# Kernel optimization log

Measured on AMD Instinct MI355X. Metric: run time of the kernel, lower is better.

Reference implementation:

```python
import jax, jax.numpy as jnp
import numpy as np

T, E = 8192, 1024
LAYER_DEPTH, NUM_LAYERS = 12, 24


def _init_params():
    ratio_0_to_1 = LAYER_DEPTH / (NUM_LAYERS - 1)
    ratio_1_to_almost_0 = 1.0 - LAYER_DEPTH / NUM_LAYERS
    zigzag = 0.5 * (jnp.arange(1, E + 1) % 3 - 1)
    time_first = jnp.full(E, jnp.log(0.3), dtype=jnp.float32) + zigzag.astype(jnp.float32)
    h = jnp.arange(0, E, dtype=jnp.float32)
    time_decay = (-5 + 8 * (h / (E - 1)) ** (0.7 + 1.3 * ratio_0_to_1)).astype(jnp.float32)
    xr = jnp.arange(E, dtype=jnp.float32) / E
    time_mix_k = jnp.power(xr, ratio_1_to_almost_0)
    time_mix_v = time_mix_k + 0.3 * ratio_0_to_1
    time_mix_r = jnp.power(xr, 0.5 * ratio_1_to_almost_0)
    return time_first, time_decay, time_mix_k, time_mix_v, time_mix_r


def setup_inputs() -> dict:
    key = jax.random.key(0)
    kx, kk_, kv_, kr_, ko_ = jax.random.split(key, 5)
    scale = 1.0 / np.sqrt(E)
    tf, td, tmk, tmv, tmr = _init_params()
    return {
        "x": jax.random.normal(kx, (T, E), dtype=jnp.float32),
        "sx": jnp.zeros((E,), jnp.float32),
        "aa": jnp.zeros((E,), jnp.float32),
        "bb": jnp.zeros((E,), jnp.float32),
        "pp": jnp.zeros((E,), jnp.float32),
        "time_first": tf,
        "time_decay": td,
        "time_mix_k": tmk,
        "time_mix_v": tmv,
        "time_mix_r": tmr,
        "Wk": jax.random.normal(kk_, (E, E), jnp.float32) * scale,
        "Wv": jax.random.normal(kv_, (E, E), jnp.float32) * scale,
        "Wr": jax.random.normal(kr_, (E, E), jnp.float32) * scale,
        "Wo": jax.random.normal(ko_, (E, E), jnp.float32) * scale,
    }


def reference(x, sx, aa, bb, pp, time_first, time_decay,
              time_mix_k, time_mix_v, time_mix_r, Wk, Wv, Wr, Wo):
    # token-shift: previous token (or carried state sx at t=0)  [T, E]
    sx_seq = jnp.concatenate((sx[None, :], x[:-1, :]), axis=0)
    kx = x * time_mix_k + sx_seq * (1.0 - time_mix_k)
    vx = x * time_mix_v + sx_seq * (1.0 - time_mix_v)
    rx = x * time_mix_r + sx_seq * (1.0 - time_mix_r)

    r = jax.nn.sigmoid(rx @ Wr)  # [T, E]
    k = kx @ Wk                  # [T, E]
    v = vx @ Wv                  # [T, E]
    decay = -jnp.exp(time_decay)  # [E]

    def step(state, kv):
        aa_, bb_, pp_ = state
        kk, vv = kv
        ww = time_first + kk
        p = jnp.maximum(pp_, ww)
        e1 = jnp.exp(pp_ - p)
        e2 = jnp.exp(ww - p)
        out = (e1 * aa_ + e2 * vv) / (e1 * bb_ + e2)
        ww2 = decay + pp_
        p2 = jnp.maximum(ww2, kk)
        e1b = jnp.exp(ww2 - p2)
        e2b = jnp.exp(kk - p2)
        return (e1b * aa_ + e2b * vv, e1b * bb_ + e2b, p2), out

    (aa_f, bb_f, pp_f), wkv = jax.lax.scan(step, (aa, bb, pp), (k, v))
    out = x + (r * wkv) @ Wo
    return out, x[-1, :], aa_f, bb_f, pp_f
```

## Files before the change

kernel.cpp:

```cpp
#include <hip/hip_runtime.h>
#include <cstdint>
#include <cstddef>

typedef __bf16 bf16x8 __attribute__((ext_vector_type(8)));
typedef float  f32x4  __attribute__((ext_vector_type(4)));

#define TT 8192
#define EE 1024
#define LDSK 40

__device__ __forceinline__ unsigned short f2bf(float f) {
    union { float f; unsigned int u; } v; v.f = f;
    unsigned int r = v.u + 0x7FFFu + ((v.u >> 16) & 1u);
    return (unsigned short)(r >> 16);
}
__device__ __forceinline__ float b2f(unsigned int h) {
    union { unsigned int u; float f; } v; v.u = h << 16; return v.f;
}
__device__ __forceinline__ void gload_lds16(const void* g, void* l) {
    __builtin_amdgcn_global_load_lds((__attribute__((address_space(1))) void*)g,
                                     (__attribute__((address_space(3))) void*)l, 16, 0, 0);
}

__global__ void wt_kernel(const float* __restrict__ Wk, const float* __restrict__ Wv,
                          const float* __restrict__ Wr, const float* __restrict__ Wo,
                          unsigned short* __restrict__ Tk, unsigned short* __restrict__ Tv,
                          unsigned short* __restrict__ Tr, unsigned short* __restrict__ To) {
    __shared__ float tile[32][33];
    const float* W; unsigned short* D;
    switch (blockIdx.z) {
        case 0:  W = Wk; D = Tk; break;
        case 1:  W = Wv; D = Tv; break;
        case 2:  W = Wr; D = Tr; break;
        default: W = Wo; D = To; break;
    }
    const int bx = blockIdx.x * 32, by = blockIdx.y * 32;
    const int tx = threadIdx.x, ty = threadIdx.y;
#pragma unroll
    for (int r = 0; r < 4; ++r)
        tile[ty + 8 * r][tx] = W[(size_t)(by + ty + 8 * r) * EE + bx + tx];
    __syncthreads();
#pragma unroll
    for (int r = 0; r < 4; ++r)
        D[(size_t)(bx + ty + 8 * r) * EE + by + tx] = f2bf(tile[tx][ty + 8 * r]);
}

__global__ void prep_kernel(const float* __restrict__ Wk, const float* __restrict__ Wv,
                            const float* __restrict__ Wr, const float* __restrict__ Wo,
                            unsigned short* __restrict__ Tk, unsigned short* __restrict__ Tv,
                            unsigned short* __restrict__ Tr, unsigned short* __restrict__ To,
                            const float* __restrict__ x, const float* __restrict__ sx,
                            const float* __restrict__ tmk, const float* __restrict__ tmv,
                            const float* __restrict__ tmr,
                            unsigned short* __restrict__ kxb, unsigned short* __restrict__ vxb,
                            unsigned short* __restrict__ rxb) {
    const int bid = blockIdx.x;
    if (bid < 4096) {
        __shared__ float tile[32][33];
        const int z = bid >> 10;
        const float* W; unsigned short* D;
        switch (z) {
            case 0:  W = Wk; D = Tk; break;
            case 1:  W = Wv; D = Tv; break;
            case 2:  W = Wr; D = Tr; break;
            default: W = Wo; D = To; break;
        }
        const int by = ((bid >> 5) & 31) * 32, bx = (bid & 31) * 32;
        const int tx = threadIdx.x & 31, ty = threadIdx.x >> 5;
#pragma unroll
        for (int r = 0; r < 4; ++r)
            tile[ty + 8 * r][tx] = W[(size_t)(by + ty + 8 * r) * EE + bx + tx];
        __syncthreads();
#pragma unroll
        for (int r = 0; r < 4; ++r)
            D[(size_t)(bx + ty + 8 * r) * EE + by + tx] = f2bf(tile[tx][ty + 8 * r]);
    } else {
        const int gid  = (bid - 4096) * 256 + threadIdx.x;
        const int base = gid * 4;
        const int t = base >> 10;
        const int e = base & (EE - 1);
        float4 xv = *(const float4*)(x + base);
        float4 pv = (t > 0) ? *(const float4*)(x + base - EE) : *(const float4*)(sx + e);
        float4 mk = *(const float4*)(tmk + e);
        float4 mv = *(const float4*)(tmv + e);
        float4 mr = *(const float4*)(tmr + e);
        ushort4 ko, vo, ro;
        ko.x = f2bf(fmaf(mk.x, xv.x - pv.x, pv.x));
        ko.y = f2bf(fmaf(mk.y, xv.y - pv.y, pv.y));
        ko.z = f2bf(fmaf(mk.z, xv.z - pv.z, pv.z));
        ko.w = f2bf(fmaf(mk.w, xv.w - pv.w, pv.w));
        vo.x = f2bf(fmaf(mv.x, xv.x - pv.x, pv.x));
        vo.y = f2bf(fmaf(mv.y, xv.y - pv.y, pv.y));
        vo.z = f2bf(fmaf(mv.z, xv.z - pv.z, pv.z));
        vo.w = f2bf(fmaf(mv.w, xv.w - pv.w, pv.w));
        ro.x = f2bf(fmaf(mr.x, xv.x - pv.x, pv.x));
        ro.y = f2bf(fmaf(mr.y, xv.y - pv.y, pv.y));
        ro.z = f2bf(fmaf(mr.z, xv.z - pv.z, pv.z));
        ro.w = f2bf(fmaf(mr.w, xv.w - pv.w, pv.w));
        *(ushort4*)(kxb + base) = ko;
        *(ushort4*)(vxb + base) = vo;
        *(ushort4*)(rxb + base) = ro;
    }
}

__global__ __launch_bounds__(256, 4) void gemm_kvr3(
        const unsigned short* __restrict__ kxb, const unsigned short* __restrict__ vxb,
        const unsigned short* __restrict__ rxb,
        const unsigned short* __restrict__ Wkt, const unsigned short* __restrict__ Wvt,
        const unsigned short* __restrict__ Wrt,
        unsigned short* __restrict__ kf, unsigned short* __restrict__ vf,
        unsigned short* __restrict__ ry) {
    __shared__ __align__(16) unsigned short As[128 * 64];
    __shared__ __align__(16) unsigned short Bs[128 * 64];
    const int z = blockIdx.z;
    const unsigned short* A  = (z == 0) ? kxb : (z == 1) ? vxb : rxb;
    const unsigned short* Bt = (z == 0) ? Wkt : (z == 1) ? Wvt : Wrt;
    unsigned short* C        = (z == 0) ? kf  : (z == 1) ? vf  : ry;

    const int tid  = threadIdx.x;
    const int wave = tid >> 6, lane = tid & 63;
    const int wm = (wave >> 1) * 64, wn = (wave & 1) * 64;
    const int l15 = lane & 15, lq = lane >> 4;
    const int lrow = lane >> 3;
    const int lcolg = (((lane & 7) ^ lrow) & 7) * 8;
    const int sw = l15 & 7;
    const int bm = blockIdx.x * 128, bn = blockIdx.y * 128;

    f32x4 acc[4][4] = {};

    for (int kt = 0; kt < 1024; kt += 64) {
        __syncthreads();
#pragma unroll
        for (int p = 0; p < 4; ++p) {
            const int r0 = p * 32 + wave * 8;
            gload_lds16(A  + (size_t)(bm + r0 + lrow) * 1024 + kt + lcolg, &As[r0 * 64]);
            gload_lds16(Bt + (size_t)(bn + r0 + lrow) * 1024 + kt + lcolg, &Bs[r0 * 64]);
        }
        __syncthreads();
#pragma unroll
        for (int h = 0; h < 2; ++h) {
            bf16x8 af[4], bfr[4];
#pragma unroll
            for (int i = 0; i < 4; ++i) {
                const int g = ((h * 4 + lq) ^ sw) * 8;
                af[i]  = *(const bf16x8*)(&As[(wm + i * 16 + l15) * 64 + g]);
                bfr[i] = *(const bf16x8*)(&Bs[(wn + i * 16 + l15) * 64 + g]);
            }
#pragma unroll
            for (int i = 0; i < 4; ++i)
#pragma unroll
                for (int j = 0; j < 4; ++j)
                    acc[i][j] = __builtin_amdgcn_mfma_f32_16x16x32_bf16(af[i], bfr[j], acc[i][j], 0, 0, 0);
        }
    }

    const bool sig = (z == 2);
#pragma unroll
    for (int i = 0; i < 4; ++i)
#pragma unroll
        for (int j = 0; j < 4; ++j) {
            const int col = bn + wn + j * 16 + l15;
#pragma unroll
            for (int r = 0; r < 4; ++r) {
                const int row = bm + wm + i * 16 + lq * 4 + r;
                float val = acc[i][j][r];
                if (sig) val = 1.f / (1.f + __expf(-val));
                C[(size_t)row * 1024 + col] = f2bf(val);
            }
        }
}

__global__ __launch_bounds__(256, 4) void gemm_wo(const unsigned short* __restrict__ A,
                                                  const unsigned short* __restrict__ Bt,
                                                  const float* __restrict__ Res,
                                                  float* __restrict__ C) {
    __shared__ __align__(16) unsigned short As[128 * 64];
    __shared__ __align__(16) unsigned short Bs[128 * 64];
    const int tid  = threadIdx.x;
    const int wave = tid >> 6, lane = tid & 63;
    const int wm = (wave >> 1) * 64, wn = (wave & 1) * 64;
    const int l15 = lane & 15, lq = lane >> 4;
    const int lrow = lane >> 3;
    const int lcolg = (((lane & 7) ^ lrow) & 7) * 8;
    const int sw = l15 & 7;
    const int bm = blockIdx.x * 128, bn = blockIdx.y * 128;

    f32x4 acc[4][4] = {};

    for (int kt = 0; kt < 1024; kt += 64) {
        __syncthreads();
#pragma unroll
        for (int p = 0; p < 4; ++p) {
            const int r0 = p * 32 + wave * 8;
            gload_lds16(A  + (size_t)(bm + r0 + lrow) * 1024 + kt + lcolg, &As[r0 * 64]);
            gload_lds16(Bt + (size_t)(bn + r0 + lrow) * 1024 + kt + lcolg, &Bs[r0 * 64]);
        }
        __syncthreads();
#pragma unroll
        for (int h = 0; h < 2; ++h) {
            bf16x8 af[4], bfr[4];
#pragma unroll
            for (int i = 0; i < 4; ++i) {
                const int g = ((h * 4 + lq) ^ sw) * 8;
                af[i]  = *(const bf16x8*)(&As[(wm + i * 16 + l15) * 64 + g]);
                bfr[i] = *(const bf16x8*)(&Bs[(wn + i * 16 + l15) * 64 + g]);
            }
#pragma unroll
            for (int i = 0; i < 4; ++i)
#pragma unroll
                for (int j = 0; j < 4; ++j)
                    acc[i][j] = __builtin_amdgcn_mfma_f32_16x16x32_bf16(af[i], bfr[j], acc[i][j], 0, 0, 0);
        }
    }

#pragma unroll
    for (int i = 0; i < 4; ++i)
#pragma unroll
        for (int j = 0; j < 4; ++j) {
            const int col = bn + wn + j * 16 + l15;
#pragma unroll
            for (int r = 0; r < 4; ++r) {
                const int row = bm + wm + i * 16 + lq * 4 + r;
                const size_t idx = (size_t)row * 1024 + col;
                C[idx] = acc[i][j][r] + Res[idx];
            }
        }
}

template <int NC>
__global__ void wkv_pass_a(const unsigned short* __restrict__ k,
                           const unsigned short* __restrict__ v,
                           const float* __restrict__ td,
                           float* __restrict__ Sa, float* __restrict__ Sb, float* __restrict__ Sp) {
    const int CL = TT / NC;
    const int gid = blockIdx.x * 256 + threadIdx.x;
    const int c  = gid >> 8;
    const int e0 = (gid & 255) * 4;
    const float4 tdv = *(const float4*)(td + e0);
    float w[4] = { -__expf(tdv.x), -__expf(tdv.y), -__expf(tdv.z), -__expf(tdv.w) };
    float sa[4] = {0.f, 0.f, 0.f, 0.f}, sb[4] = {0.f, 0.f, 0.f, 0.f};
    float sp[4] = {-1e30f, -1e30f, -1e30f, -1e30f};
    const size_t base = (size_t)c * CL * EE + e0;
#pragma unroll
    for (int i = 0; i < CL; ++i) {
        const ushort4 k4 = *(const ushort4*)(k + base + (size_t)i * EE);
        const ushort4 v4 = *(const ushort4*)(v + base + (size_t)i * EE);
        const unsigned short ks[4] = {k4.x, k4.y, k4.z, k4.w};
        const unsigned short vs[4] = {v4.x, v4.y, v4.z, v4.w};
        const float fi = (float)(CL - 1 - i);
#pragma unroll
        for (int j = 0; j < 4; ++j) {
            const float kk = b2f(ks[j]), vv = b2f(vs[j]);
            const float q  = fmaf(w[j], fi, kk);
            const float p2 = fmaxf(sp[j], q);
            const float e1 = __expf(sp[j] - p2), e2 = __expf(q - p2);
            sa[j] = fmaf(e1, sa[j], e2 * vv);
            sb[j] = fmaf(e1, sb[j], e2);
            sp[j] = p2;
        }
    }
#pragma unroll
    for (int j = 0; j < 4; ++j) {
        Sa[c * EE + e0 + j] = sa[j];
        Sb[c * EE + e0 + j] = sb[j];
        Sp[c * EE + e0 + j] = sp[j];
    }
}

template <int NC>
__global__ void wkv_pass_b_par(const float* __restrict__ aa, const float* __restrict__ bb,
                               const float* __restrict__ pp, const float* __restrict__ td,
                               const float* __restrict__ x,
                               const float* __restrict__ Sa, const float* __restrict__ Sb,
                               const float* __restrict__ Sp,
                               float* __restrict__ ina, float* __restrict__ inb,
                               float* __restrict__ inp, float* __restrict__ outTail) {
    const int CL = TT / NC;
    const int e = blockIdx.x, c = threadIdx.x;
    __shared__ float sA[NC], sB[NC], sP[NC];
    const float w = -__expf(td[e]);

    float a = Sa[c * EE + e], b = Sb[c * EE + e], p = Sp[c * EE + e];

    for (int s = 1; s < NC; s <<= 1) {
        sA[c] = a; sB[c] = b; sP[c] = p;
        __syncthreads();
        if (c >= s) {
            const float myLen = (float)(CL * min(c + 1, s));
            const float aL = sA[c - s], bL = sB[c - s], pL = sP[c - s];
            const float pLd = pL + w * myLen;
            const float pn  = fmaxf(pLd, p);
            const float e1  = __expf(pLd - pn), e2 = __expf(p - pn);
            a = fmaf(e1, aL, e2 * a);
            b = fmaf(e1, bL, e2 * b);
            p = pn;
        }
        __syncthreads();
    }

    sA[c] = a; sB[c] = b; sP[c] = p;
    __syncthreads();

    const float a0 = aa[e], b0 = bb[e], p0 = pp[e];
    float ea, eb, ep;
    if (c == 0) { ea = a0; eb = b0; ep = p0; }
    else {
        const float aL = sA[c - 1], bL = sB[c - 1], pL = sP[c - 1];
        const float p0d = p0 + w * (float)(c * CL);
        const float pn  = fmaxf(p0d, pL);
        const float e1  = __expf(p0d - pn), e2 = __expf(pL - pn);
        ea = fmaf(e1, a0, e2 * aL);
        eb = fmaf(e1, b0, e2 * bL);
        ep = pn;
    }
    ina[e * NC + c] = ea; inb[e * NC + c] = eb; inp[e * NC + c] = ep;

    if (c == NC - 1) {
        const float p0d = p0 + w * (float)TT;
        const float pn  = fmaxf(p0d, p);
        const float e1  = __expf(p0d - pn), e2 = __expf(p - pn);
        outTail[e]          = x[(size_t)(TT - 1) * EE + e];
        outTail[EE + e]     = fmaf(e1, a0, e2 * a);
        outTail[2 * EE + e] = fmaf(e1, b0, e2 * b);
        outTail[3 * EE + e] = pn;
    }
}

template <int NC>
__global__ void wkv_pass_c(const unsigned short* __restrict__ k,
                           const unsigned short* __restrict__ v,
                           const float* __restrict__ tf, const float* __restrict__ td,
                           const float* __restrict__ ina, const float* __restrict__ inb,
                           const float* __restrict__ inp,
                           unsigned short* ry) {
    const int CL = TT / NC;
    const int gid = blockIdx.x * 256 + threadIdx.x;
    const int c  = gid >> 8;
    const int e0 = (gid & 255) * 4;
    const float4 tdv = *(const float4*)(td + e0);
    const float4 tfv = *(const float4*)(tf + e0);
    float w[4] = { -__expf(tdv.x), -__expf(tdv.y), -__expf(tdv.z), -__expf(tdv.w) };
    float u[4] = { tfv.x, tfv.y, tfv.z, tfv.w };
    float a[4], b[4], p[4];
#pragma unroll
    for (int j = 0; j < 4; ++j) {
        a[j] = ina[(e0 + j) * NC + c];
        b[j] = inb[(e0 + j) * NC + c];
        p[j] = inp[(e0 + j) * NC + c];
    }
    const size_t base = (size_t)c * CL * EE + e0;
#pragma unroll 4
    for (int i = 0; i < CL; ++i) {
        const size_t idx = base + (size_t)i * EE;
        const ushort4 k4 = *(const ushort4*)(k + idx);
        const ushort4 v4 = *(const ushort4*)(v + idx);
        const ushort4 r4 = *(const ushort4*)(ry + idx);
        const unsigned short ks[4] = {k4.x, k4.y, k4.z, k4.w};
        const unsigned short vs[4] = {v4.x, v4.y, v4.z, v4.w};
        const unsigned short rs[4] = {r4.x, r4.y, r4.z, r4.w};
        unsigned short os[4];
#pragma unroll
        for (int j = 0; j < 4; ++j) {
            const float kk = b2f(ks[j]), vv = b2f(vs[j]), rr = b2f(rs[j]);
            const float ww = u[j] + kk;
            const float pq = fmaxf(p[j], ww);
            const float e1 = __expf(p[j] - pq), e2 = __expf(ww - pq);
            const float wkv = fmaf(e1, a[j], e2 * vv) * __builtin_amdgcn_rcpf(fmaf(e1, b[j], e2));
            os[j] = f2bf(rr * wkv);
            const float ww2 = w[j] + p[j];
            const float p2  = fmaxf(ww2, kk);
            const float e1b = __expf(ww2 - p2), e2b = __expf(kk - p2);
            a[j] = fmaf(e1b, a[j], e2b * vv);
            b[j] = fmaf(e1b, b[j], e2b);
            p[j] = p2;
        }
        ushort4 o4;
        o4.x = os[0]; o4.y = os[1]; o4.z = os[2]; o4.w = os[3];
        *(ushort4*)(ry + idx) = o4;
    }
}

__global__ void wkv_pass_b_small(const float* __restrict__ aa, const float* __restrict__ bb,
                                 const float* __restrict__ pp, const float* __restrict__ td,
                                 const float* __restrict__ x,
                                 const float* __restrict__ Sa, const float* __restrict__ Sb,
                                 const float* __restrict__ Sp,
                                 float* __restrict__ ina, float* __restrict__ inb,
                                 float* __restrict__ inp, float* __restrict__ outTail) {
    const int NC = 128, CL = TT / NC;
    const int e = blockIdx.x * 256 + threadIdx.x;
    const float w  = -__expf(td[e]);
    const float wL = w * (float)CL;
    float a = aa[e], b = bb[e], p = pp[e];
    for (int c = 0; c < NC; ++c) {
        ina[e * NC + c] = a; inb[e * NC + c] = b; inp[e * NC + c] = p;
        const int idx = c * EE + e;
        const float sa = Sa[idx], sb = Sb[idx], sp = Sp[idx];
        const float pw = p + wL;
        const float p2 = fmaxf(pw, sp);
        const float e1 = __expf(pw - p2), e2 = __expf(sp - p2);
        a = fmaf(e1, a, e2 * sa);
        b = fmaf(e1, b, e2 * sb);
        p = p2;
    }
    outTail[e]          = x[(size_t)(TT - 1) * EE + e];
    outTail[EE + e]     = a;
    outTail[2 * EE + e] = b;
    outTail[3 * EE + e] = p;
}

__global__ __launch_bounds__(256, 4) void gemm_kvr(
        const float* __restrict__ X, const float* __restrict__ SX,
        const float* __restrict__ tmk, const float* __restrict__ tmv,
        const float* __restrict__ tmr,
        const unsigned short* __restrict__ Wkt, const unsigned short* __restrict__ Wvt,
        const unsigned short* __restrict__ Wrt,
        unsigned short* __restrict__ outK, unsigned short* __restrict__ outV,
        unsigned short* __restrict__ outR) {
    __shared__ __align__(16) unsigned short As[128 * LDSK];
    __shared__ __align__(16) unsigned short Bs[128 * LDSK];
    const int z = blockIdx.z;
    const float* TM = (z == 0) ? tmk : (z == 1) ? tmv : tmr;
    const unsigned short* Bt = (z == 0) ? Wkt : (z == 1) ? Wvt : Wrt;
    unsigned short* Cout = (z == 0) ? outK : (z == 1) ? outV : outR;

    const int tid  = threadIdx.x;
    const int wave = tid >> 6, lane = tid & 63;
    const int wm = (wave >> 1) * 64, wn = (wave & 1) * 64;
    const int l15 = lane & 15, lq = lane >> 4;
    const int bm = blockIdx.x * 128, bn = blockIdx.y * 128;

    f32x4 acc[4][4] = {};

    for (int kt = 0; kt < 1024; kt += 32) {
        __syncthreads();
#pragma unroll
        for (int p = 0; p < 2; ++p) {
            const int li  = p * 256 + tid;
            const int row = li >> 2, q = li & 3;
            const int e0  = kt + q * 8;
            {
                const int t = bm + row;
                const float* xr = X + (size_t)t * EE + e0;
                const float* pr = (t > 0) ? (X + (size_t)(t - 1) * EE + e0) : (SX + e0);
                float4 xa = *(const float4*)xr, xb = *(const float4*)(xr + 4);
                float4 pa = *(const float4*)pr, pb = *(const float4*)(pr + 4);
                float4 ma = *(const float4*)(TM + e0), mb = *(const float4*)(TM + e0 + 4);
                ushort4 lo, hi;
                lo.x = f2bf(fmaf(ma.x, xa.x - pa.x, pa.x));
                lo.y = f2bf(fmaf(ma.y, xa.y - pa.y, pa.y));
                lo.z = f2bf(fmaf(ma.z, xa.z - pa.z, pa.z));
                lo.w = f2bf(fmaf(ma.w, xa.w - pa.w, pa.w));
                hi.x = f2bf(fmaf(mb.x, xb.x - pb.x, pb.x));
                hi.y = f2bf(fmaf(mb.y, xb.y - pb.y, pb.y));
                hi.z = f2bf(fmaf(mb.z, xb.z - pb.z, pb.z));
                hi.w = f2bf(fmaf(mb.w, xb.w - pb.w, pb.w));
                *(ushort4*)(&As[row * LDSK + q * 8])     = lo;
                *(ushort4*)(&As[row * LDSK + q * 8 + 4]) = hi;
            }
            *(uint4*)(&Bs[row * LDSK + q * 8]) =
                *(const uint4*)(Bt + (size_t)(bn + row) * 1024 + e0);
        }
        __syncthreads();
        bf16x8 af[4], bfr[4];
#pragma unroll
        for (int i = 0; i < 4; ++i) {
            af[i]  = *(const bf16x8*)(&As[(wm + i * 16 + l15) * LDSK + lq * 8]);
            bfr[i] = *(const bf16x8*)(&Bs[(wn + i * 16 + l15) * LDSK + lq * 8]);
        }
#pragma unroll
        for (int i = 0; i < 4; ++i)
#pragma unroll
            for (int j = 0; j < 4; ++j)
                acc[i][j] = __builtin_amdgcn_mfma_f32_16x16x32_bf16(af[i], bfr[j], acc[i][j], 0, 0, 0);
    }

    const bool sig = (z == 2);
#pragma unroll
    for (int i = 0; i < 4; ++i)
#pragma unroll
        for (int j = 0; j < 4; ++j) {
            const int col = bn + wn + j * 16 + l15;
#pragma unroll
            for (int r = 0; r < 4; ++r) {
                const int row = bm + wm + i * 16 + lq * 4 + r;
                float val = acc[i][j][r];
                if (sig) val = 1.f / (1.f + __expf(-val));
                Cout[(size_t)row * 1024 + col] = f2bf(val);
            }
        }
}

extern "C" void kernel_launch(void* const* d_in, const int* in_sizes, int n_in,
                              void* d_out, int out_size, void* d_ws, size_t ws_size,
                              hipStream_t stream) {
    const float* x   = (const float*)d_in[0];
    const float* sx  = (const float*)d_in[1];
    const float* aa  = (const float*)d_in[2];
    const float* bb  = (const float*)d_in[3];
    const float* pp  = (const float*)d_in[4];
    const float* tf  = (const float*)d_in[5];
    const float* td  = (const float*)d_in[6];
    const float* tmk = (const float*)d_in[7];
    const float* tmv = (const float*)d_in[8];
    const float* tmr = (const float*)d_in[9];
    const float* Wk  = (const float*)d_in[10];
    const float* Wv  = (const float*)d_in[11];
    const float* Wr  = (const float*)d_in[12];
    const float* Wo  = (const float*)d_in[13];
    float* out = (float*)d_out;

    char* ws = (char*)d_ws;
    const size_t MB = 1ull << 20;

    unsigned short* Wkt = (unsigned short*)(ws + 0 * MB);
    unsigned short* Wvt = (unsigned short*)(ws + 2 * MB);
    unsigned short* Wrt = (unsigned short*)(ws + 4 * MB);
    unsigned short* Wot = (unsigned short*)(ws + 6 * MB);

    if (ws_size >= 75 * MB) {
        unsigned short* rxb = (unsigned short*)(ws + 8 * MB);
        unsigned short* kf  = (unsigned short*)(ws + 24 * MB);
        unsigned short* ry  = (unsigned short*)(ws + 40 * MB);
        unsigned short* vf  = (unsigned short*)(ws + 56 * MB);
        float* Sa  = (float*)(ws + 8  * MB);
        float* Sb  = (float*)(ws + 10 * MB);
        float* Sp  = (float*)(ws + 12 * MB);
        float* ina = (float*)(ws + 14 * MB);
        float* inb = (float*)(ws + 16 * MB);
        float* inp = (float*)(ws + 18 * MB);
        unsigned short* kxb = (unsigned short*)d_out;
        unsigned short* vxb = (unsigned short*)d_out + (size_t)TT * EE;

        prep_kernel<<<12288, 256, 0, stream>>>(Wk, Wv, Wr, Wo, Wkt, Wvt, Wrt, Wot,
                                               x, sx, tmk, tmv, tmr, kxb, vxb, rxb);
        gemm_kvr3<<<dim3(64, 8, 3), 256, 0, stream>>>(kxb, vxb, rxb, Wkt, Wvt, Wrt,
                                                      kf, vf, ry);
        wkv_pass_a<512><<<512, 256, 0, stream>>>(kf, vf, td, Sa, Sb, Sp);
        wkv_pass_b_par<512><<<EE, 512, 0, stream>>>(aa, bb, pp, td, x, Sa, Sb, Sp,
                                                    ina, inb, inp, out + (size_t)TT * EE);
        wkv_pass_c<512><<<512, 256, 0, stream>>>(kf, vf, tf, td,
                                                 ina, inb, inp, ry);
        gemm_wo<<<dim3(64, 8), 256, 0, stream>>>(ry, Wot, x, out);
    } else {
        unsigned short* ry = (unsigned short*)(ws + 8 * MB);
        char* scan = ws + 24 * MB;
        const size_t QK = (size_t)128 * EE * sizeof(float);
        float* Sa  = (float*)(scan);
        float* Sb  = (float*)(scan + QK);
        float* Sp  = (float*)(scan + 2 * QK);
        float* ina = (float*)(scan + 3 * QK);
        float* inb = (float*)(scan + 4 * QK);
        float* inp = (float*)(scan + 5 * QK);
        unsigned short* kf = (unsigned short*)d_out;
        unsigned short* vf = (unsigned short*)d_out + (size_t)TT * EE;

        wt_kernel<<<dim3(32, 32, 4), dim3(32, 8), 0, stream>>>(Wk, Wv, Wr, Wo, Wkt, Wvt, Wrt, Wot);
        gemm_kvr<<<dim3(64, 8, 3), 256, 0, stream>>>(x, sx, tmk, tmv, tmr,
                                                     Wkt, Wvt, Wrt, kf, vf, ry);
        wkv_pass_a<128><<<128, 256, 0, stream>>>(kf, vf, td, Sa, Sb, Sp);
        wkv_pass_b_small<<<4, 256, 0, stream>>>(aa, bb, pp, td, x, Sa, Sb, Sp,
                                                ina, inb, inp, out + (size_t)TT * EE);
        wkv_pass_c<128><<<128, 256, 0, stream>>>(kf, vf, tf, td,
                                                 ina, inb, inp, ry);
        gemm_wo<<<dim3(64, 8), 256, 0, stream>>>(ry, Wot, x, out);
    }
}
```

Before: 257.0 us.

## Fuse three WKV scan passes into one cooperative kernel with grid sync

Replaces the three chunked-scan kernels (local chunk reduction, cross-chunk prefix, chunk replay) with one cooperative kernel that uses grid-wide syncs between phases. The k/v chunk is kept in LDS so the replay phase does not reload it from global memory. The prefix phase now has each block handle two channels with a 256-thread scan over paired chunks. This removes two launches and the k/v re-read, at the cost of two grid barriers and 64KB of LDS per block, which limits residency and requires all 512 blocks to be co-resident.

```diff
diff --git a/kernel.cpp b/kernel.cpp
--- a/kernel.cpp
+++ b/kernel.cpp
@@ -1,6 +1,9 @@
 #include <hip/hip_runtime.h>
+#include <hip/hip_cooperative_groups.h>
 #include <cstdint>
 #include <cstddef>
+
+namespace cg = cooperative_groups;
 
 typedef __bf16 bf16x8 __attribute__((ext_vector_type(8)));
 typedef float  f32x4  __attribute__((ext_vector_type(4)));
@@ -227,6 +230,180 @@
         }
 }
 
+__global__ __launch_bounds__(256, 2) void wkv_fused(
+        const unsigned short* __restrict__ kf, const unsigned short* __restrict__ vf,
+        const float* __restrict__ aa, const float* __restrict__ bb,
+        const float* __restrict__ pp, const float* __restrict__ tf,
+        const float* __restrict__ td, const float* __restrict__ x,
+        unsigned short* __restrict__ ry,
+        float* __restrict__ Sa, float* __restrict__ Sb, float* __restrict__ Sp,
+        float* __restrict__ ina, float* __restrict__ inb, float* __restrict__ inp,
+        float* __restrict__ outTail) {
+    const int NC = 512, CL = 16;
+    __shared__ __align__(16) unsigned short kL[16 * EE];
+    __shared__ __align__(16) unsigned short vL[16 * EE];
+    __shared__ float sA[256], sB[256], sP[256];
+    const int c = blockIdx.x, tid = threadIdx.x;
+    const int e0 = tid * 4;
+
+    const float4 tdv = *(const float4*)(td + e0);
+    float w4[4] = { -__expf(tdv.x), -__expf(tdv.y), -__expf(tdv.z), -__expf(tdv.w) };
+    float sa[4] = {0.f, 0.f, 0.f, 0.f}, sb[4] = {0.f, 0.f, 0.f, 0.f};
+    float sp[4] = {-1e30f, -1e30f, -1e30f, -1e30f};
+    const size_t gbase = (size_t)c * CL * EE + e0;
+#pragma unroll
+    for (int i = 0; i < CL; ++i) {
+        const ushort4 k4 = *(const ushort4*)(kf + gbase + (size_t)i * EE);
+        const ushort4 v4 = *(const ushort4*)(vf + gbase + (size_t)i * EE);
+        *(ushort4*)(kL + i * EE + e0) = k4;
+        *(ushort4*)(vL + i * EE + e0) = v4;
+        const unsigned short ks[4] = {k4.x, k4.y, k4.z, k4.w};
+        const unsigned short vs[4] = {v4.x, v4.y, v4.z, v4.w};
+        const float fi = (float)(CL - 1 - i);
+#pragma unroll
+        for (int j = 0; j < 4; ++j) {
+            const float kk = b2f(ks[j]), vv = b2f(vs[j]);
+            const float q  = fmaf(w4[j], fi, kk);
+            const float p2 = fmaxf(sp[j], q);
+            const float e1 = __expf(sp[j] - p2), e2 = __expf(q - p2);
+            sa[j] = fmaf(e1, sa[j], e2 * vv);
+            sb[j] = fmaf(e1, sb[j], e2);
+            sp[j] = p2;
+        }
+    }
+#pragma unroll
+    for (int j = 0; j < 4; ++j) {
+        Sa[(size_t)(e0 + j) * NC + c] = sa[j];
+        Sb[(size_t)(e0 + j) * NC + c] = sb[j];
+        Sp[(size_t)(e0 + j) * NC + c] = sp[j];
+    }
+    __threadfence();
+    cg::this_grid().sync();
+
+    for (int ch = 0; ch < 2; ++ch) {
+        const int e = 2 * c + ch;
+        const float w = -__expf(td[e]);
+        const float2 a2 = *(const float2*)(Sa + (size_t)e * NC + 2 * tid);
+        const float2 b2 = *(const float2*)(Sb + (size_t)e * NC + 2 * tid);
+        const float2 p2 = *(const float2*)(Sp + (size_t)e * NC + 2 * tid);
+        const float eA = a2.x, eB = b2.x, eP = p2.x;
+        float Pa, Pb, Pp;
+        {
+            const float pl = p2.x + w * (float)CL;
+            const float pn = fmaxf(pl, p2.y);
+            const float x1 = __expf(pl - pn), x2 = __expf(p2.y - pn);
+            Pa = fmaf(x1, a2.x, x2 * a2.y);
+            Pb = fmaf(x1, b2.x, x2 * b2.y);
+            Pp = pn;
+        }
+        for (int s = 1; s < 256; s <<= 1) {
+            sA[tid] = Pa; sB[tid] = Pb; sP[tid] = Pp;
+            __syncthreads();
+            if (tid >= s) {
+                const float pL = sP[tid - s] + w * (float)(CL * 2 * s);
+                const float pn = fmaxf(pL, Pp);
+                const float x1 = __expf(pL - pn), x2 = __expf(Pp - pn);
+                Pa = fmaf(x1, sA[tid - s], x2 * Pa);
+                Pb = fmaf(x1, sB[tid - s], x2 * Pb);
+                Pp = pn;
+            }
+            __syncthreads();
+        }
+        sA[tid] = Pa; sB[tid] = Pb; sP[tid] = Pp;
+        __syncthreads();
+
+        const float a0 = aa[e], b0 = bb[e], p0 = pp[e];
+        {
+            const int cc = 2 * tid;
+            float ea, eb, ep;
+            if (tid == 0) { ea = a0; eb = b0; ep = p0; }
+            else {
+                const float aP = sA[tid - 1], bP = sB[tid - 1], pP = sP[tid - 1];
+                const float p0d = p0 + w * (float)(cc * CL);
+                const float pn  = fmaxf(p0d, pP);
+                const float x1  = __expf(p0d - pn), x2 = __expf(pP - pn);
+                ea = fmaf(x1, a0, x2 * aP);
+                eb = fmaf(x1, b0, x2 * bP);
+                ep = pn;
+            }
+            ina[(size_t)cc * EE + e] = ea;
+            inb[(size_t)cc * EE + e] = eb;
+            inp[(size_t)cc * EE + e] = ep;
+        }
+        {
+            float qa, qb, qp;
+            if (tid == 0) { qa = eA; qb = eB; qp = eP; }
+            else {
+                const float pL = sP[tid - 1] + w * (float)CL;
+                const float pn = fmaxf(pL, eP);
+                const float x1 = __expf(pL - pn), x2 = __expf(eP - pn);
+                qa = fmaf(x1, sA[tid - 1], x2 * eA);
+                qb = fmaf(x1, sB[tid - 1], x2 * eB);
+                qp = pn;
+            }
+            const int cc = 2 * tid + 1;
+            const float p0d = p0 + w * (float)(cc * CL);
+            const float pn  = fmaxf(p0d, qp);
+            const float x1  = __expf(p0d - pn), x2 = __expf(qp - pn);
+            ina[(size_t)cc * EE + e] = fmaf(x1, a0, x2 * qa);
+            inb[(size_t)cc * EE + e] = fmaf(x1, b0, x2 * qb);
+            inp[(size_t)cc * EE + e] = pn;
+        }
+        if (tid == 255) {
+            const float p0d = p0 + w * (float)TT;
+            const float pn  = fmaxf(p0d, Pp);
+            const float x1  = __expf(p0d - pn), x2 = __expf(Pp - pn);
+            outTail[e]          = x[(size_t)(TT - 1) * EE + e];
+            outTail[EE + e]     = fmaf(x1, a0, x2 * Pa);
+            outTail[2 * EE + e] = fmaf(x1, b0, x2 * Pb);
+            outTail[3 * EE + e] = pn;
+        }
+        __syncthreads();
+    }
+    __threadfence();
+    cg::this_grid().sync();
+
+    const float4 tfv = *(const float4*)(tf + e0);
+    const float u[4] = { tfv.x, tfv.y, tfv.z, tfv.w };
+    float a[4], b[4], p[4];
+    {
+        const float4 av = *(const float4*)(ina + (size_t)c * EE + e0);
+        const float4 bv = *(const float4*)(inb + (size_t)c * EE + e0);
+        const float4 pv = *(const float4*)(inp + (size_t)c * EE + e0);
+        a[0] = av.x; a[1] = av.y; a[2] = av.z; a[3] = av.w;
+        b[0] = bv.x; b[1] = bv.y; b[2] = bv.z; b[3] = bv.w;
+        p[0] = pv.x; p[1] = pv.y; p[2] = pv.z; p[3] = pv.w;
+    }
+#pragma unroll 4
+    for (int i = 0; i < CL; ++i) {
+        const ushort4 k4 = *(const ushort4*)(kL + i * EE + e0);
+        const ushort4 v4 = *(const ushort4*)(vL + i * EE + e0);
+        const ushort4 r4 = *(const ushort4*)(ry + gbase + (size_t)i * EE);
+        const unsigned short ks[4] = {k4.x, k4.y, k4.z, k4.w};
+        const unsigned short vs[4] = {v4.x, v4.y, v4.z, v4.w};
+        const unsigned short rs[4] = {r4.x, r4.y, r4.z, r4.w};
+        unsigned short os[4];
+#pragma unroll
+        for (int j = 0; j < 4; ++j) {
+            const float kk = b2f(ks[j]), vv = b2f(vs[j]), rr = b2f(rs[j]);
+            const float ww = u[j] + kk;
+            const float pq = fmaxf(p[j], ww);
+            const float e1 = __expf(p[j] - pq), e2 = __expf(ww - pq);
+            const float wkv = fmaf(e1, a[j], e2 * vv) * __builtin_amdgcn_rcpf(fmaf(e1, b[j], e2));
+            os[j] = f2bf(rr * wkv);
+            const float ww2 = w4[j] + p[j];
+            const float pz  = fmaxf(ww2, kk);
+            const float e1b = __expf(ww2 - pz), e2b = __expf(kk - pz);
+            a[j] = fmaf(e1b, a[j], e2b * vv);
+            b[j] = fmaf(e1b, b[j], e2b);
+            p[j] = pz;
+        }
+        ushort4 o4;
+        o4.x = os[0]; o4.y = os[1]; o4.z = os[2]; o4.w = os[3];
+        *(ushort4*)(ry + gbase + (size_t)i * EE) = o4;
+    }
+}
+
 template <int NC>
 __global__ void wkv_pass_a(const unsigned short* __restrict__ k,
                            const unsigned short* __restrict__ v,
@@ -264,119 +441,6 @@
         Sa[c * EE + e0 + j] = sa[j];
         Sb[c * EE + e0 + j] = sb[j];
         Sp[c * EE + e0 + j] = sp[j];
-    }
-}
-
-template <int NC>
-__global__ void wkv_pass_b_par(const float* __restrict__ aa, const float* __restrict__ bb,
-                               const float* __restrict__ pp, const float* __restrict__ td,
-                               const float* __restrict__ x,
-                               const float* __restrict__ Sa, const float* __restrict__ Sb,
-                               const float* __restrict__ Sp,
-                               float* __restrict__ ina, float* __restrict__ inb,
-                               float* __restrict__ inp, float* __restrict__ outTail) {
-    const int CL = TT / NC;
-    const int e = blockIdx.x, c = threadIdx.x;
-    __shared__ float sA[NC], sB[NC], sP[NC];
-    const float w = -__expf(td[e]);
-
-    float a = Sa[c * EE + e], b = Sb[c * EE + e], p = Sp[c * EE + e];
-
-    for (int s = 1; s < NC; s <<= 1) {
-        sA[c] = a; sB[c] = b; sP[c] = p;
-        __syncthreads();
-        if (c >= s) {
-            const float myLen = (float)(CL * min(c + 1, s));
-            const float aL = sA[c - s], bL = sB[c - s], pL = sP[c - s];
-            const float pLd = pL + w * myLen;
-            const float pn  = fmaxf(pLd, p);
-            const float e1  = __expf(pLd - pn), e2 = __expf(p - pn);
-            a = fmaf(e1, aL, e2 * a);
-            b = fmaf(e1, bL, e2 * b);
-            p = pn;
-        }
-        __syncthreads();
-    }
-
-    sA[c] = a; sB[c] = b; sP[c] = p;
-    __syncthreads();
-
-    const float a0 = aa[e], b0 = bb[e], p0 = pp[e];
-    float ea, eb, ep;
-    if (c == 0) { ea = a0; eb = b0; ep = p0; }
-    else {
-        const float aL = sA[c - 1], bL = sB[c - 1], pL = sP[c - 1];
-        const float p0d = p0 + w * (float)(c * CL);
-        const float pn  = fmaxf(p0d, pL);
-        const float e1  = __expf(p0d - pn), e2 = __expf(pL - pn);
-        ea = fmaf(e1, a0, e2 * aL);
-        eb = fmaf(e1, b0, e2 * bL);
-        ep = pn;
-    }
-    ina[e * NC + c] = ea; inb[e * NC + c] = eb; inp[e * NC + c] = ep;
-
-    if (c == NC - 1) {
-        const float p0d = p0 + w * (float)TT;
-        const float pn  = fmaxf(p0d, p);
-        const float e1  = __expf(p0d - pn), e2 = __expf(p - pn);
-        outTail[e]          = x[(size_t)(TT - 1) * EE + e];
-        outTail[EE + e]     = fmaf(e1, a0, e2 * a);
-        outTail[2 * EE + e] = fmaf(e1, b0, e2 * b);
-        outTail[3 * EE + e] = pn;
-    }
-}
-
-template <int NC>
-__global__ void wkv_pass_c(const unsigned short* __restrict__ k,
-                           const unsigned short* __restrict__ v,
-                           const float* __restrict__ tf, const float* __restrict__ td,
-                           const float* __restrict__ ina, const float* __restrict__ inb,
-                           const float* __restrict__ inp,
-                           unsigned short* ry) {
-    const int CL = TT / NC;
-    const int gid = blockIdx.x * 256 + threadIdx.x;
-    const int c  = gid >> 8;
-    const int e0 = (gid & 255) * 4;
-    const float4 tdv = *(const float4*)(td + e0);
-    const float4 tfv = *(const float4*)(tf + e0);
-    float w[4] = { -__expf(tdv.x), -__expf(tdv.y), -__expf(tdv.z), -__expf(tdv.w) };
-    float u[4] = { tfv.x, tfv.y, tfv.z, tfv.w };
-    float a[4], b[4], p[4];
-#pragma unroll
-    for (int j = 0; j < 4; ++j) {
-        a[j] = ina[(e0 + j) * NC + c];
-        b[j] = inb[(e0 + j) * NC + c];
-        p[j] = inp[(e0 + j) * NC + c];
-    }
-    const size_t base = (size_t)c * CL * EE + e0;
-#pragma unroll 4
-    for (int i = 0; i < CL; ++i) {
-        const size_t idx = base + (size_t)i * EE;
-        const ushort4 k4 = *(const ushort4*)(k + idx);
-        const ushort4 v4 = *(const ushort4*)(v + idx);
-        const ushort4 r4 = *(const ushort4*)(ry + idx);
-        const unsigned short ks[4] = {k4.x, k4.y, k4.z, k4.w};
-        const unsigned short vs[4] = {v4.x, v4.y, v4.z, v4.w};
-        const unsigned short rs[4] = {r4.x, r4.y, r4.z, r4.w};
-        unsigned short os[4];
-#pragma unroll
-        for (int j = 0; j < 4; ++j) {
-            const float kk = b2f(ks[j]), vv = b2f(vs[j]), rr = b2f(rs[j]);
-            const float ww = u[j] + kk;
-            const float pq = fmaxf(p[j], ww);
-            const float e1 = __expf(p[j] - pq), e2 = __expf(ww - pq);
-            const float wkv = fmaf(e1, a[j], e2 * vv) * __builtin_amdgcn_rcpf(fmaf(e1, b[j], e2));
-            os[j] = f2bf(rr * wkv);
-            const float ww2 = w[j] + p[j];
-            const float p2  = fmaxf(ww2, kk);
-            const float e1b = __expf(ww2 - p2), e2b = __expf(kk - p2);
-            a[j] = fmaf(e1b, a[j], e2b * vv);
-            b[j] = fmaf(e1b, b[j], e2b);
-            p[j] = p2;
-        }
-        ushort4 o4;
-        o4.x = os[0]; o4.y = os[1]; o4.z = os[2]; o4.w = os[3];
-        *(ushort4*)(ry + idx) = o4;
     }
 }
 
@@ -409,6 +473,60 @@
     outTail[3 * EE + e] = p;
 }
 
+template <int NC>
+__global__ void wkv_pass_c(const unsigned short* __restrict__ k,
+                           const unsigned short* __restrict__ v,
+                           const float* __restrict__ tf, const float* __restrict__ td,
+                           const float* __restrict__ ina, const float* __restrict__ inb,
+                           const float* __restrict__ inp,
+                           unsigned short* ry) {
+    const int CL = TT / NC;
+    const int gid = blockIdx.x * 256 + threadIdx.x;
+    const int c  = gid >> 8;
+    const int e0 = (gid & 255) * 4;
+    const float4 tdv = *(const float4*)(td + e0);
+    const float4 tfv = *(const float4*)(tf + e0);
+    float w[4] = { -__expf(tdv.x), -__expf(tdv.y), -__expf(tdv.z), -__expf(tdv.w) };
+    float u[4] = { tfv.x, tfv.y, tfv.z, tfv.w };
+    float a[4], b[4], p[4];
+#pragma unroll
+    for (int j = 0; j < 4; ++j) {
+        a[j] = ina[(e0 + j) * NC + c];
+        b[j] = inb[(e0 + j) * NC + c];
+        p[j] = inp[(e0 + j) * NC + c];
+    }
+    const size_t base = (size_t)c * CL * EE + e0;
+#pragma unroll 4
+    for (int i = 0; i < CL; ++i) {
+        const size_t idx = base + (size_t)i * EE;
+        const ushort4 k4 = *(const ushort4*)(k + idx);
+        const ushort4 v4 = *(const ushort4*)(v + idx);
+        const ushort4 r4 = *(const ushort4*)(ry + idx);
+        const unsigned short ks[4] = {k4.x, k4.y, k4.z, k4.w};
+        const unsigned short vs[4] = {v4.x, v4.y, v4.z, v4.w};
+        const unsigned short rs[4] = {r4.x, r4.y, r4.z, r4.w};
+        unsigned short os[4];
+#pragma unroll
+        for (int j = 0; j < 4; ++j) {
+            const float kk = b2f(ks[j]), vv = b2f(vs[j]), rr = b2f(rs[j]);
+            const float ww = u[j] + kk;
+            const float pq = fmaxf(p[j], ww);
+            const float e1 = __expf(p[j] - pq), e2 = __expf(ww - pq);
+            const float wkv = fmaf(e1, a[j], e2 * vv) * __builtin_amdgcn_rcpf(fmaf(e1, b[j], e2));
+            os[j] = f2bf(rr * wkv);
+            const float ww2 = w[j] + p[j];
+            const float p2  = fmaxf(ww2, kk);
+            const float e1b = __expf(ww2 - p2), e2b = __expf(kk - p2);
+            a[j] = fmaf(e1b, a[j], e2b * vv);
+            b[j] = fmaf(e1b, b[j], e2b);
+            p[j] = p2;
+        }
+        ushort4 o4;
+        o4.x = os[0]; o4.y = os[1]; o4.z = os[2]; o4.w = os[3];
+        *(ushort4*)(ry + idx) = o4;
+    }
+}
+
 __global__ __launch_bounds__(256, 4) void gemm_kvr(
         const float* __restrict__ X, const float* __restrict__ SX,
         const float* __restrict__ tmk, const float* __restrict__ tmv,
@@ -531,16 +649,24 @@
         float* inp = (float*)(ws + 18 * MB);
         unsigned short* kxb = (unsigned short*)d_out;
         unsigned short* vxb = (unsigned short*)d_out + (size_t)TT * EE;
+        float* outTail = out + (size_t)TT * EE;
 
         prep_kernel<<<12288, 256, 0, stream>>>(Wk, Wv, Wr, Wo, Wkt, Wvt, Wrt, Wot,
                                                x, sx, tmk, tmv, tmr, kxb, vxb, rxb);
         gemm_kvr3<<<dim3(64, 8, 3), 256, 0, stream>>>(kxb, vxb, rxb, Wkt, Wvt, Wrt,
                                                       kf, vf, ry);
-        wkv_pass_a<512><<<512, 256, 0, stream>>>(kf, vf, td, Sa, Sb, Sp);
-        wkv_pass_b_par<512><<<EE, 512, 0, stream>>>(aa, bb, pp, td, x, Sa, Sb, Sp,
-                                                    ina, inb, inp, out + (size_t)TT * EE);
-        wkv_pass_c<512><<<512, 256, 0, stream>>>(kf, vf, tf, td,
-                                                 ina, inb, inp, ry);
+        {
+            const unsigned short* kfc = kf;
+            const unsigned short* vfc = vf;
+            void* args[] = {
+                (void*)&kfc, (void*)&vfc, (void*)&aa, (void*)&bb, (void*)&pp,
+                (void*)&tf, (void*)&td, (void*)&x, (void*)&ry,
+                (void*)&Sa, (void*)&Sb, (void*)&Sp,
+                (void*)&ina, (void*)&inb, (void*)&inp, (void*)&outTail
+            };
+            hipLaunchCooperativeKernel((const void*)wkv_fused, dim3(512), dim3(256),
+                                       args, 0, stream);
+        }
         gemm_wo<<<dim3(64, 8), 256, 0, stream>>>(ry, Wot, x, out);
     } else {
         unsigned short* ry = (unsigned short*)(ws + 8 * MB);
```

Measured after the change: 531.4 us. 107% more time.
